# Optimization experiments

Measured on AMD Instinct MI355X. Metric: run time of the kernel, lower is better.

The kernel has to match this reference:

```python
import jax, jax.numpy as jnp
import numpy as np

B, S, V, E, H, M, CS, U = 1, 2048, 50257, 512, 768, 256, 64, 2048


def setup_inputs() -> dict:
    key = jax.random.key(0)
    ks = jax.random.split(key, 16)
    s = 0.02
    p = {}
    p["input_ids"] = jax.random.randint(ks[0], (B, S), 0, V)
    p["untied_token_ids"] = jax.random.randint(ks[1], (U,), 0, V)
    p["emb"] = jax.random.normal(ks[2], (V, E)) * s
    p["w_ih"] = jax.random.normal(ks[3], (3 * H, E)) * s
    p["w_hh"] = jax.random.normal(ks[4], (3 * H, H)) * s
    p["b_ih"] = jnp.zeros((3 * H,))
    p["b_hh"] = jnp.zeros((3 * H,))
    p["Wq"] = jax.random.normal(ks[5], (M, H)) * s
    p["bq"] = jnp.zeros((M,))
    p["Wk"] = jax.random.normal(ks[6], (M, H)) * s
    p["bk"] = jnp.zeros((M,))
    p["Whf"] = jax.random.normal(ks[7], (4 * E, H)) * s
    p["bhf"] = jnp.zeros((4 * E,))
    p["Whp"] = jax.random.normal(ks[8], (E, 4 * E)) * s
    p["bhp"] = jnp.zeros((E,))
    p["Wcv"] = jax.random.normal(ks[9], (E, H)) * s
    p["bcv"] = jnp.zeros((E,))
    p["Wph"] = jax.random.normal(ks[10], (U, E)) * s
    p["bph"] = jnp.zeros((U,))
    p["out_bias"] = jnp.zeros((V,))
    return p


def gru(x, w_ih, w_hh, b_ih, b_hh):
    # x: [B, S, E] -> states [B, S, H]; PyTorch GRU gate order (r, z, n)
    Hh = w_hh.shape[1]

    def step(h, xt):
        gx = xt @ w_ih.T + b_ih
        gh = h @ w_hh.T + b_hh
        xr, xz, xn = jnp.split(gx, 3, axis=-1)
        hr, hz, hn = jnp.split(gh, 3, axis=-1)
        r = jax.nn.sigmoid(xr + hr)
        z = jax.nn.sigmoid(xz + hz)
        n = jnp.tanh(xn + r * hn)
        h = (1.0 - z) * n + z * h
        return h, h

    h0 = jnp.zeros((x.shape[0], Hh), x.dtype)
    _, hs = jax.lax.scan(step, h0, jnp.swapaxes(x, 0, 1))
    return jnp.swapaxes(hs, 0, 1)


def reference(input_ids, untied_token_ids, emb, w_ih, w_hh, b_ih, b_hh, Wq, bq, Wk, bk, Whf, bhf, Whp, bhp, Wcv, bcv, Wph, bph, out_bias):
    x = emb[input_ids]                                  # [B,S,E]
    states = gru(x, w_ih, w_hh, b_ih, b_hh)             # [B,S,H] (dropout=0, eval)
    head = jnp.square(jax.nn.relu(states @ Whf.T + bhf))  # [B,S,4E]
    base_feat = head @ Whp.T + bhp                      # [B,S,E]
    base_logits = base_feat @ emb.T + out_bias          # [B,S,V]

    nc = S // CS  # S == max_length, divisible by chunk_size -> pad_len = 0
    chunked = states.reshape(B, nc, CS, H).mean(axis=2)  # [B,nc,H]
    qk = states @ Wq.T + bq                              # [B,S,M]
    mk = chunked @ Wk.T + bk                             # [B,nc,M]
    scores = jnp.einsum('bsm,bcm->bsc', qk, mk) / jnp.sqrt(jnp.asarray(M, qk.dtype))

    chunk_ends = jnp.minimum(jnp.arange(nc) * CS + (CS - 1), S - 1)
    mask = chunk_ends[None, None, :] < jnp.arange(S)[None, :, None]  # [1,S,nc]
    neg = jnp.finfo(scores.dtype).min
    scores = jnp.where(mask, scores, neg)
    attn = jax.nn.softmax(scores, axis=-1) * mask
    attn = attn / jnp.clip(attn.sum(axis=-1, keepdims=True), 1e-6)

    base_partial = base_feat @ Wph.T + bph               # [B,S,U]
    chunk_partial = (chunked @ Wcv.T + bcv) @ Wph.T + bph  # [B,nc,U]
    mem_partial = jnp.einsum('bsc,bcu->bsu', attn, chunk_partial)
    total_partial = base_partial + mem_partial           # [B,S,U]

    # scatter_add partial logits into full-vocab logits (duplicates accumulate)
    return base_logits.at[:, :, untied_token_ids].add(total_partial)
```

## Files before the change

### kernel.cpp

```cpp
#include <hip/hip_runtime.h>
#include <hip/hip_bf16.h>
#include <math.h>

#define SEQ   2048
#define VOC   50257
#define EMB   512
#define HID   768
#define G3    2304
#define MDIM  256
#define CSZ   64
#define NCHUNK 32
#define UDIM  2048
#define E4    2048

#define G_GRU 48
#define CANARY 0xFFFFFFFFu

typedef uint32_t u32x4  __attribute__((ext_vector_type(4)));
typedef float    f32x4  __attribute__((ext_vector_type(4)));
typedef short    s16x8  __attribute__((ext_vector_type(8)));
typedef __bf16   bf16x8 __attribute__((ext_vector_type(8)));

__global__ __launch_bounds__(256) void cvt_f32_bf16(const float* __restrict__ src,
                                                    __bf16* __restrict__ dst, int n8) {
    int stride = gridDim.x * 256;
    for (int i = blockIdx.x * 256 + threadIdx.x; i < n8; i += stride) {
        const float4* s = reinterpret_cast<const float4*>(src + (size_t)i * 8);
        float4 a = s[0], b = s[1];
        bf16x8 o;
        o[0]=(__bf16)a.x; o[1]=(__bf16)a.y; o[2]=(__bf16)a.z; o[3]=(__bf16)a.w;
        o[4]=(__bf16)b.x; o[5]=(__bf16)b.y; o[6]=(__bf16)b.z; o[7]=(__bf16)b.w;
        *reinterpret_cast<bf16x8*>(dst + (size_t)i * 8) = o;
    }
}

__global__ __launch_bounds__(256) void embed_kernel(const int* __restrict__ ids,
                                                    const float* __restrict__ emb,
                                                    float* __restrict__ X) {
    int s = blockIdx.x;
    int id = ids[s];
    const float* src = &emb[(size_t)id * EMB];
    float* dst = &X[(size_t)s * EMB];
    for (int i = threadIdx.x; i < EMB; i += 256) dst[i] = src[i];
}

__global__ __launch_bounds__(64) void embed16_kernel(const int* __restrict__ ids,
                                                     const __bf16* __restrict__ emb16,
                                                     __bf16* __restrict__ X16) {
    int s = blockIdx.x;
    int id = ids[s];
    const bf16x8* src = reinterpret_cast<const bf16x8*>(emb16 + (size_t)id * EMB);
    bf16x8* dst = reinterpret_cast<bf16x8*>(X16 + (size_t)s * EMB);
    int i = threadIdx.x;
    dst[i] = src[i];
}

template<int EPI>
__global__ __launch_bounds__(256) void gemm_nt(const float* __restrict__ A,
                                               const float* __restrict__ B,
                                               const float* __restrict__ bias,
                                               float* __restrict__ C,
                                               int M, int N, int K) {
    __shared__ float As[16][132];
    __shared__ float Bs[16][132];
    const int tid = threadIdx.x;
    const int tx = tid & 15;
    const int ty = tid >> 4;
    const int m0 = blockIdx.y * 128;
    const int n0 = blockIdx.x * 128;

    float acc[8][8];
    #pragma unroll
    for (int i = 0; i < 8; i++)
        #pragma unroll
        for (int j = 0; j < 8; j++) acc[i][j] = 0.f;

    for (int k0 = 0; k0 < K; k0 += 16) {
        #pragma unroll
        for (int i = 0; i < 2; i++) {
            int idx = tid * 2 + i;
            int r   = idx >> 2;
            int c4  = idx & 3;
            float4 av = {0.f, 0.f, 0.f, 0.f};
            float4 bv = {0.f, 0.f, 0.f, 0.f};
            int ar = m0 + r;
            if (ar < M) av = *reinterpret_cast<const float4*>(&A[(size_t)ar * K + k0 + c4 * 4]);
            int br = n0 + r;
            if (br < N) bv = *reinterpret_cast<const float4*>(&B[(size_t)br * K + k0 + c4 * 4]);
            As[c4 * 4 + 0][r] = av.x; As[c4 * 4 + 1][r] = av.y;
            As[c4 * 4 + 2][r] = av.z; As[c4 * 4 + 3][r] = av.w;
            Bs[c4 * 4 + 0][r] = bv.x; Bs[c4 * 4 + 1][r] = bv.y;
            Bs[c4 * 4 + 2][r] = bv.z; Bs[c4 * 4 + 3][r] = bv.w;
        }
        __syncthreads();
        #pragma unroll
        for (int k = 0; k < 16; k++) {
            float4 a0 = *reinterpret_cast<const float4*>(&As[k][ty * 4]);
            float4 a1 = *reinterpret_cast<const float4*>(&As[k][64 + ty * 4]);
            float4 b0 = *reinterpret_cast<const float4*>(&Bs[k][tx * 4]);
            float4 b1 = *reinterpret_cast<const float4*>(&Bs[k][64 + tx * 4]);
            float a[8] = {a0.x, a0.y, a0.z, a0.w, a1.x, a1.y, a1.z, a1.w};
            float b[8] = {b0.x, b0.y, b0.z, b0.w, b1.x, b1.y, b1.z, b1.w};
            #pragma unroll
            for (int i = 0; i < 8; i++)
                #pragma unroll
                for (int j = 0; j < 8; j++)
                    acc[i][j] = fmaf(a[i], b[j], acc[i][j]);
        }
        __syncthreads();
    }

    #pragma unroll
    for (int i = 0; i < 8; i++) {
        int r = m0 + ((i < 4) ? (ty * 4 + i) : (64 + ty * 4 + (i - 4)));
        if (r >= M) continue;
        #pragma unroll
        for (int j = 0; j < 8; j++) {
            int c = n0 + ((j < 4) ? (tx * 4 + j) : (64 + tx * 4 + (j - 4)));
            if (c >= N) continue;
            float v = acc[i][j] + bias[c];
            if (EPI == 1) { v = fmaxf(v, 0.f); v = v * v; }
            C[(size_t)r * N + c] = v;
        }
    }
}

template<int EPI>
__global__ __launch_bounds__(256) void gemm_bt16(const __bf16* __restrict__ A,
                                                 const __bf16* __restrict__ B,
                                                 const float* __restrict__ bias,
                                                 float* __restrict__ C,
                                                 int M, int N, int K) {
    constexpr int LDT = 40;
    __shared__ __bf16 As[128 * LDT];
    __shared__ __bf16 Bs[128 * LDT];
    const int tid  = threadIdx.x;
    const int lane = tid & 63;
    const int wave = tid >> 6;
    const int wm = wave >> 1;
    const int wn = wave & 1;
    const int m0 = blockIdx.y * 128;
    const int n0 = blockIdx.x * 128;
    const int l15 = lane & 15;
    const int l4  = lane >> 4;

    f32x4 acc[4][4];
    #pragma unroll
    for (int i = 0; i < 4; i++)
        #pragma unroll
        for (int j = 0; j < 4; j++) acc[i][j] = (f32x4){0.f, 0.f, 0.f, 0.f};

    const int r  = tid >> 1;
    const int hf = tid & 1;

    for (int k0 = 0; k0 < K; k0 += 32) {
        const __bf16* ap = &A[(size_t)(m0 + r) * K + k0 + hf * 16];
        s16x8 av0 = *reinterpret_cast<const s16x8*>(ap);
        s16x8 av1 = *reinterpret_cast<const s16x8*>(ap + 8);
        s16x8 bv0, bv1;
        #pragma unroll
        for (int q = 0; q < 8; q++) { bv0[q] = 0; bv1[q] = 0; }
        int bn = n0 + r;
        if (bn < N) {
            const __bf16* bp = &B[(size_t)bn * K + k0 + hf * 16];
            bv0 = *reinterpret_cast<const s16x8*>(bp);
            bv1 = *reinterpret_cast<const s16x8*>(bp + 8);
        }
        __syncthreads();
        *reinterpret_cast<s16x8*>(&As[r * LDT + hf * 16])     = av0;
        *reinterpret_cast<s16x8*>(&As[r * LDT + hf * 16 + 8]) = av1;
        *reinterpret_cast<s16x8*>(&Bs[r * LDT + hf * 16])     = bv0;
        *reinterpret_cast<s16x8*>(&Bs[r * LDT + hf * 16 + 8]) = bv1;
        __syncthreads();

        s16x8 af[4], bf[4];
        #pragma unroll
        for (int i = 0; i < 4; i++)
            af[i] = *reinterpret_cast<const s16x8*>(&As[(wm * 64 + i * 16 + l15) * LDT + l4 * 8]);
        #pragma unroll
        for (int j = 0; j < 4; j++)
            bf[j] = *reinterpret_cast<const s16x8*>(&Bs[(wn * 64 + j * 16 + l15) * LDT + l4 * 8]);
        #pragma unroll
        for (int i = 0; i < 4; i++)
            #pragma unroll
            for (int j = 0; j < 4; j++)
                acc[i][j] = __builtin_amdgcn_mfma_f32_16x16x32_bf16(af[i], bf[j], acc[i][j], 0, 0, 0);
    }

    #pragma unroll
    for (int j = 0; j < 4; j++) {
        int col = n0 + wn * 64 + j * 16 + l15;
        if (col >= N) continue;
        float bv = bias[col];
        #pragma unroll
        for (int i = 0; i < 4; i++) {
            int row = m0 + wm * 64 + i * 16 + l4 * 4;
            #pragma unroll
            for (int q = 0; q < 4; q++) {
                float v = acc[i][j][q] + bv;
                if (EPI == 1) { v = fmaxf(v, 0.f); v = v * v; }
                C[(size_t)(row + q) * N + col] = v;
            }
        }
    }
}

__global__ __launch_bounds__(256) void gemm_bf16_logits(const float* __restrict__ A,
                                                        const float* __restrict__ B,
                                                        const float* __restrict__ bias,
                                                        float* __restrict__ C,
                                                        int M, int N, int K) {
    constexpr int LDT = 40;
    __shared__ __bf16 As[128 * LDT];
    __shared__ __bf16 Bs[128 * LDT];
    const int tid  = threadIdx.x;
    const int lane = tid & 63;
    const int wave = tid >> 6;
    const int wm = wave >> 1;
    const int wn = wave & 1;
    const int m0 = blockIdx.y * 128;
    const int n0 = blockIdx.x * 128;
    const int l15 = lane & 15;
    const int l4  = lane >> 4;

    f32x4 acc[4][4];
    #pragma unroll
    for (int i = 0; i < 4; i++)
        #pragma unroll
        for (int j = 0; j < 4; j++) acc[i][j] = (f32x4){0.f, 0.f, 0.f, 0.f};

    const int r  = tid >> 1;
    const int hf = tid & 1;

    for (int k0 = 0; k0 < K; k0 += 32) {
        const float* ap = &A[(size_t)(m0 + r) * K + k0 + hf * 16];
        float4 a0 = *reinterpret_cast<const float4*>(ap);
        float4 a1 = *reinterpret_cast<const float4*>(ap + 4);
        float4 a2 = *reinterpret_cast<const float4*>(ap + 8);
        float4 a3 = *reinterpret_cast<const float4*>(ap + 12);
        int bn = n0 + r;
        float4 b0 = {0,0,0,0}, b1 = {0,0,0,0}, b2 = {0,0,0,0}, b3 = {0,0,0,0};
        if (bn < N) {
            const float* bp = &B[(size_t)bn * K + k0 + hf * 16];
            b0 = *reinterpret_cast<const float4*>(bp);
            b1 = *reinterpret_cast<const float4*>(bp + 4);
            b2 = *reinterpret_cast<const float4*>(bp + 8);
            b3 = *reinterpret_cast<const float4*>(bp + 12);
        }
        __syncthreads();
        {
            __bf16* da = &As[r * LDT + hf * 16];
            bf16x8 w0, w1;
            w0[0]=(__bf16)a0.x; w0[1]=(__bf16)a0.y; w0[2]=(__bf16)a0.z; w0[3]=(__bf16)a0.w;
            w0[4]=(__bf16)a1.x; w0[5]=(__bf16)a1.y; w0[6]=(__bf16)a1.z; w0[7]=(__bf16)a1.w;
            w1[0]=(__bf16)a2.x; w1[1]=(__bf16)a2.y; w1[2]=(__bf16)a2.z; w1[3]=(__bf16)a2.w;
            w1[4]=(__bf16)a3.x; w1[5]=(__bf16)a3.y; w1[6]=(__bf16)a3.z; w1[7]=(__bf16)a3.w;
            *reinterpret_cast<bf16x8*>(da)     = w0;
            *reinterpret_cast<bf16x8*>(da + 8) = w1;
            __bf16* db = &Bs[r * LDT + hf * 16];
            bf16x8 v0, v1;
            v0[0]=(__bf16)b0.x; v0[1]=(__bf16)b0.y; v0[2]=(__bf16)b0.z; v0[3]=(__bf16)b0.w;
            v0[4]=(__bf16)b1.x; v0[5]=(__bf16)b1.y; v0[6]=(__bf16)b1.z; v0[7]=(__bf16)b1.w;
            v1[0]=(__bf16)b2.x; v1[1]=(__bf16)b2.y; v1[2]=(__bf16)b2.z; v1[3]=(__bf16)b2.w;
            v1[4]=(__bf16)b3.x; v1[5]=(__bf16)b3.y; v1[6]=(__bf16)b3.z; v1[7]=(__bf16)b3.w;
            *reinterpret_cast<bf16x8*>(db)     = v0;
            *reinterpret_cast<bf16x8*>(db + 8) = v1;
        }
        __syncthreads();

        s16x8 af[4], bf[4];
        #pragma unroll
        for (int i = 0; i < 4; i++)
            af[i] = *reinterpret_cast<const s16x8*>(&As[(wm * 64 + i * 16 + l15) * LDT + l4 * 8]);
        #pragma unroll
        for (int j = 0; j < 4; j++)
            bf[j] = *reinterpret_cast<const s16x8*>(&Bs[(wn * 64 + j * 16 + l15) * LDT + l4 * 8]);
        #pragma unroll
        for (int i = 0; i < 4; i++)
            #pragma unroll
            for (int j = 0; j < 4; j++)
                acc[i][j] = __builtin_amdgcn_mfma_f32_16x16x32_bf16(af[i], bf[j], acc[i][j], 0, 0, 0);
    }

    #pragma unroll
    for (int j = 0; j < 4; j++) {
        int col = n0 + wn * 64 + j * 16 + l15;
        if (col >= N) continue;
        float bv = bias[col];
        #pragma unroll
        for (int i = 0; i < 4; i++) {
            int row = m0 + wm * 64 + i * 16 + l4 * 4;
            #pragma unroll
            for (int q = 0; q < 4; q++)
                C[(size_t)(row + q) * N + col] = acc[i][j][q] + bv;
        }
    }
}

__device__ __forceinline__ float fast_sigmoid(float x) {
    x = fminf(fmaxf(x, -30.f), 30.f);
    return __builtin_amdgcn_rcpf(1.f + __expf(-x));
}
__device__ __forceinline__ float fast_tanh(float x) {
    x = fminf(fmaxf(x, -15.f), 15.f);
    float e = __expf(2.f * x);
    return (e - 1.f) * __builtin_amdgcn_rcpf(e + 1.f);
}

__global__ __launch_bounds__(256, 1) void gru_kernel(const float* __restrict__ GX,
                                                     const float* __restrict__ Whh,
                                                     const float* __restrict__ bhh,
                                                     float* __restrict__ states) {
    __shared__ float h_s[HID];
    const int tid  = threadIdx.x;
    const int g    = blockIdx.x;
    const int tx   = tid & 15;
    const int ty   = tid >> 4;
    const int gu   = g * 16 + ty;
    const int wave = tid >> 6;
    const int lane = tid & 63;

    float4 W4[3][12];
    #pragma unroll
    for (int p = 0; p < 3; p++) {
        const float* wr = &Whh[(size_t)(p * HID + gu) * HID + 4 * tx];
        #pragma unroll
        for (int j = 0; j < 12; j++)
            W4[p][j] = *reinterpret_cast<const float4*>(&wr[64 * j]);
    }
    float bh[3];
    #pragma unroll
    for (int p = 0; p < 3; p++) bh[p] = bhh[p * HID + gu];

    float hv  = 0.f;
    float gx0 = GX[0 * HID + gu];
    float gx1 = GX[1 * HID + gu];
    float gx2 = GX[2 * HID + gu];

    for (int t = 0; t < SEQ; t++) {
        float ngx0 = 0.f, ngx1 = 0.f, ngx2 = 0.f;
        if (t + 1 < SEQ) {
            const float* gp = &GX[(size_t)(t + 1) * G3];
            ngx0 = gp[0 * HID + gu];
            ngx1 = gp[1 * HID + gu];
            ngx2 = gp[2 * HID + gu];
        }

        float4 h4[12];
        if (t > 0) {
            if (tid < 192) {
                const float* pp = states + (size_t)(t - 1) * HID + tid * 4;
                u32x4 q;
                float s;
                do {
                    asm volatile(
                        "global_load_dwordx4 %0, %1, off sc0 sc1\n\t"
                        "s_waitcnt vmcnt(0)"
                        : "=&v"(q) : "v"(pp) : "memory");
                    f32x4 f = __builtin_bit_cast(f32x4, q);
                    s = f[0] + f[1] + f[2] + f[3];
                } while (s != s);
                *reinterpret_cast<u32x4*>(&h_s[tid * 4]) = q;
            }
            __syncthreads();
            #pragma unroll
            for (int j = 0; j < 12; j++)
                h4[j] = *reinterpret_cast<const float4*>(&h_s[4 * tx + 64 * j]);
        } else {
            #pragma unroll
            for (int j = 0; j < 12; j++) h4[j] = make_float4(0.f, 0.f, 0.f, 0.f);
        }

        float accp[3];
        #pragma unroll
        for (int p = 0; p < 3; p++) {
            float a = 0.f;
            #pragma unroll
            for (int j = 0; j < 12; j++) {
                a = fmaf(W4[p][j].x, h4[j].x, a);
                a = fmaf(W4[p][j].y, h4[j].y, a);
                a = fmaf(W4[p][j].z, h4[j].z, a);
                a = fmaf(W4[p][j].w, h4[j].w, a);
            }
            accp[p] = a;
        }
        #pragma unroll
        for (int p = 0; p < 3; p++) {
            accp[p] += __shfl_xor(accp[p], 1);
            accp[p] += __shfl_xor(accp[p], 2);
            accp[p] += __shfl_xor(accp[p], 4);
            accp[p] += __shfl_xor(accp[p], 8);
        }

        float r = fast_sigmoid(gx0 + accp[0] + bh[0]);
        float z = fast_sigmoid(gx1 + accp[1] + bh[1]);
        float n = fast_tanh(gx2 + r * (accp[2] + bh[2]));
        hv = (1.f - z) * n + z * hv;

        float v0 = __shfl(hv, 0);
        float v1 = __shfl(hv, 16);
        float v2 = __shfl(hv, 32);
        float v3 = __shfl(hv, 48);
        if (lane == 0) {
            f32x4 pv = {v0, v1, v2, v3};
            float* dp = states + (size_t)t * HID + g * 16 + wave * 4;
            asm volatile(
                "global_store_dwordx4 %0, %1, off sc0 sc1"
                :: "v"(dp), "v"(pv) : "memory");
        }
        gx0 = ngx0; gx1 = ngx1; gx2 = ngx2;
    }
}

__global__ __launch_bounds__(256) void chunkmean_kernel(const float* __restrict__ states,
                                                        float* __restrict__ chunked) {
    int c = blockIdx.x;
    for (int e = threadIdx.x; e < HID; e += 256) {
        float s = 0.f;
        #pragma unroll 8
        for (int i = 0; i < CSZ; i++)
            s += states[(size_t)(c * CSZ + i) * HID + e];
        chunked[c * HID + e] = s * (1.f / 64.f);
    }
}

__global__ void attn_kernel(const float* __restrict__ qk,
                            const float* __restrict__ mk,
                            float* __restrict__ attn) {
    int s = blockIdx.x;
    int lane = threadIdx.x;
    int c = lane & 31;
    int h = lane >> 5;
    const float* q = &qk[(size_t)s * MDIM];
    const float* m = &mk[(size_t)c * MDIM];
    float sc = 0.f;
    for (int k = h; k < MDIM; k += 2) sc = fmaf(q[k], m[k], sc);
    sc += __shfl_xor(sc, 32);
    sc *= (1.0f / 16.0f);
    bool allowed = (CSZ * c + (CSZ - 1)) < s;
    float v = allowed ? sc : -3.4e38f;
    float mx = v;
    #pragma unroll
    for (int d = 16; d >= 1; d >>= 1) mx = fmaxf(mx, __shfl_xor(mx, d));
    float e = (allowed && mx > -1e37f) ? expf(sc - mx) : 0.f;
    float sm = e;
    #pragma unroll
    for (int d = 16; d >= 1; d >>= 1) sm += __shfl_xor(sm, d);
    float a = (sm > 0.f) ? e / sm : 0.f;
    if (lane < 32) attn[(size_t)s * NCHUNK + c] = a;
}

__global__ __launch_bounds__(256) void total_scatter_kernel(const float* __restrict__ bp,
                                                            const float* __restrict__ cp,
                                                            const float* __restrict__ attn,
                                                            const int* __restrict__ uids,
                                                            float* __restrict__ out) {
    int s = blockIdx.x;
    __shared__ float a_s[NCHUNK];
    if (threadIdx.x < NCHUNK) a_s[threadIdx.x] = attn[(size_t)s * NCHUNK + threadIdx.x];
    __syncthreads();
    for (int u = threadIdx.x; u < UDIM; u += 256) {
        float t = bp[(size_t)s * UDIM + u];
        #pragma unroll 8
        for (int c = 0; c < NCHUNK; c++)
            t = fmaf(a_s[c], cp[(size_t)c * UDIM + u], t);
        atomicAdd(&out[(size_t)s * VOC + uids[u]], t);
    }
}

static inline int cvt_grid(int n8) {
    int g = (n8 + 255) / 256;
    return g > 2048 ? 2048 : g;
}

extern "C" void kernel_launch(void* const* d_in, const int* in_sizes, int n_in,
                              void* d_out, int out_size, void* d_ws, size_t ws_size,
                              hipStream_t stream) {
    const int*   ids   = (const int*)d_in[0];
    const int*   uids  = (const int*)d_in[1];
    const float* emb   = (const float*)d_in[2];
    const float* w_ih  = (const float*)d_in[3];
    const float* w_hh  = (const float*)d_in[4];
    const float* b_ih  = (const float*)d_in[5];
    const float* b_hh  = (const float*)d_in[6];
    const float* Wq    = (const float*)d_in[7];
    const float* bq    = (const float*)d_in[8];
    const float* Wk    = (const float*)d_in[9];
    const float* bk    = (const float*)d_in[10];
    const float* Whf   = (const float*)d_in[11];
    const float* bhf   = (const float*)d_in[12];
    const float* Whp   = (const float*)d_in[13];
    const float* bhp   = (const float*)d_in[14];
    const float* Wcv   = (const float*)d_in[15];
    const float* bcv   = (const float*)d_in[16];
    const float* Wph   = (const float*)d_in[17];
    const float* bph   = (const float*)d_in[18];
    const float* obias = (const float*)d_in[19];
    float* out = (float*)d_out;
    float* wsf = (float*)d_ws;

    size_t off = 0;
    float* GX     = wsf + off; off += (size_t)SEQ * G3;
    float* states = wsf + off; off += (size_t)SEQ * HID;
    float* head   = wsf + off; off += (size_t)SEQ * E4;
    float* bfeat  = wsf + off; off += (size_t)SEQ * EMB;
    float* chunk  = wsf + off; off += (size_t)NCHUNK * HID;
    float* qk     = wsf + off; off += (size_t)SEQ * MDIM;
    float* mk     = wsf + off; off += (size_t)NCHUNK * MDIM;
    float* cv     = wsf + off; off += (size_t)NCHUNK * EMB;
    float* cp     = wsf + off; off += (size_t)NCHUNK * UDIM;
    float* bp     = wsf + off; off += (size_t)SEQ * UDIM;
    float* attn   = wsf + off; off += (size_t)SEQ * NCHUNK;
    size_t common_off = off;

    __bf16* X16     = (__bf16*)(wsf + off); off += (size_t)SEQ * EMB / 2;
    __bf16* emb16   = (__bf16*)(wsf + off); off += (size_t)VOC * EMB / 2;
    __bf16* wih16   = (__bf16*)(wsf + off); off += (size_t)G3 * EMB / 2;
    __bf16* Whp16   = (__bf16*)(wsf + off); off += (size_t)EMB * E4 / 2;
    __bf16* Wph16   = (__bf16*)(wsf + off); off += (size_t)UDIM * EMB / 2;
    __bf16* head16  = (__bf16*)(wsf + off); off += (size_t)SEQ * E4 / 2;
    __bf16* bfeat16 = (__bf16*)(wsf + off); off += (size_t)SEQ * EMB / 2;
    const bool big = ws_size >= off * sizeof(float);

    if (big) {
        cvt_f32_bf16<<<cvt_grid(VOC * EMB / 8), 256, 0, stream>>>(emb, emb16, VOC * EMB / 8);
        cvt_f32_bf16<<<cvt_grid(G3 * EMB / 8), 256, 0, stream>>>(w_ih, wih16, G3 * EMB / 8);
        cvt_f32_bf16<<<cvt_grid(EMB * E4 / 8), 256, 0, stream>>>(Whp, Whp16, EMB * E4 / 8);
        cvt_f32_bf16<<<cvt_grid(UDIM * EMB / 8), 256, 0, stream>>>(Wph, Wph16, UDIM * EMB / 8);
        embed16_kernel<<<SEQ, 64, 0, stream>>>(ids, emb16, X16);
        hipMemsetAsync(states, 0xFF, (size_t)SEQ * HID * sizeof(float), stream);
        gemm_bt16<0><<<dim3(G3 / 128, SEQ / 128), 256, 0, stream>>>(X16, wih16, b_ih, GX, SEQ, G3, EMB);
        gru_kernel<<<G_GRU, 256, 0, stream>>>(GX, w_hh, b_hh, states);
        chunkmean_kernel<<<NCHUNK, 256, 0, stream>>>(states, chunk);
        gemm_nt<0><<<dim3(MDIM / 128, SEQ / 128), 256, 0, stream>>>(states, Wq, bq, qk, SEQ, MDIM, HID);
        gemm_nt<0><<<dim3(MDIM / 128, 1), 256, 0, stream>>>(chunk, Wk, bk, mk, NCHUNK, MDIM, HID);
        gemm_nt<1><<<dim3(E4 / 128, SEQ / 128), 256, 0, stream>>>(states, Whf, bhf, head, SEQ, E4, HID);
        cvt_f32_bf16<<<cvt_grid(SEQ * E4 / 8), 256, 0, stream>>>(head, head16, SEQ * E4 / 8);
        gemm_bt16<0><<<dim3(EMB / 128, SEQ / 128), 256, 0, stream>>>(head16, Whp16, bhp, bfeat, SEQ, EMB, E4);
        cvt_f32_bf16<<<cvt_grid(SEQ * EMB / 8), 256, 0, stream>>>(bfeat, bfeat16, SEQ * EMB / 8);
        gemm_nt<0><<<dim3(EMB / 128, 1), 256, 0, stream>>>(chunk, Wcv, bcv, cv, NCHUNK, EMB, HID);
        gemm_nt<0><<<dim3(UDIM / 128, 1), 256, 0, stream>>>(cv, Wph, bph, cp, NCHUNK, UDIM, EMB);
        gemm_bt16<0><<<dim3(UDIM / 128, SEQ / 128), 256, 0, stream>>>(bfeat16, Wph16, bph, bp, SEQ, UDIM, EMB);
        gemm_bt16<0><<<dim3((VOC + 127) / 128, SEQ / 128), 256, 0, stream>>>(bfeat16, emb16, obias, out, SEQ, VOC, EMB);
        attn_kernel<<<SEQ, 64, 0, stream>>>(qk, mk, attn);
        total_scatter_kernel<<<SEQ, 256, 0, stream>>>(bp, cp, attn, uids, out);
    } else {
        float* X = wsf + common_off;
        embed_kernel<<<SEQ, 256, 0, stream>>>(ids, emb, X);
        hipMemsetAsync(states, 0xFF, (size_t)SEQ * HID * sizeof(float), stream);
        gemm_nt<0><<<dim3(G3 / 128, SEQ / 128), 256, 0, stream>>>(X, w_ih, b_ih, GX, SEQ, G3, EMB);
        gru_kernel<<<G_GRU, 256, 0, stream>>>(GX, w_hh, b_hh, states);
        chunkmean_kernel<<<NCHUNK, 256, 0, stream>>>(states, chunk);
        gemm_nt<0><<<dim3(MDIM / 128, SEQ / 128), 256, 0, stream>>>(states, Wq, bq, qk, SEQ, MDIM, HID);
        gemm_nt<0><<<dim3(MDIM / 128, 1), 256, 0, stream>>>(chunk, Wk, bk, mk, NCHUNK, MDIM, HID);
        gemm_nt<1><<<dim3(E4 / 128, SEQ / 128), 256, 0, stream>>>(states, Whf, bhf, head, SEQ, E4, HID);
        gemm_nt<0><<<dim3(EMB / 128, SEQ / 128), 256, 0, stream>>>(head, Whp, bhp, bfeat, SEQ, EMB, E4);
        gemm_nt<0><<<dim3(EMB / 128, 1), 256, 0, stream>>>(chunk, Wcv, bcv, cv, NCHUNK, EMB, HID);
        gemm_nt<0><<<dim3(UDIM / 128, 1), 256, 0, stream>>>(cv, Wph, bph, cp, NCHUNK, UDIM, EMB);
        gemm_nt<0><<<dim3(UDIM / 128, SEQ / 128), 256, 0, stream>>>(bfeat, Wph, bph, bp, SEQ, UDIM, EMB);
        gemm_bf16_logits<<<dim3((VOC + 127) / 128, SEQ / 128), 256, 0, stream>>>(bfeat, emb, obias, out, SEQ, VOC, EMB);
        attn_kernel<<<SEQ, 64, 0, stream>>>(qk, mk, attn);
        total_scatter_kernel<<<SEQ, 256, 0, stream>>>(bp, cp, attn, uids, out);
    }
}
```

Baseline: 5.172 ms.

## Overlap GRU recurrence with downstream head and logits GEMMs in a persistent mega-kernel

Merges the GRU recurrence, head projection, feature projection, vocab logits GEMM and base_partial GEMM into one persistent kernel. GRU blocks write states while consumer blocks poll on NaN-canary state rows and atomic stage flags, then compute 128-row stages of the downstream GEMMs as soon as their inputs are ready. Intermediate head and bfeat outputs are written directly as bf16, dropping the separate conversion kernels. The aim is to hide the serial GRU latency behind the large logits GEMM. The cost is spin-waiting, reliance on all 256 blocks being co-resident, and GEMM blocks competing with GRU blocks for bandwidth.

```diff
diff --git a/kernel.cpp b/kernel.cpp
--- a/kernel.cpp
+++ b/kernel.cpp
@@ -14,6 +14,8 @@
 #define E4    2048
 
 #define G_GRU 48
+#define NCONS 208
+#define NSTAGE 16
 #define CANARY 0xFFFFFFFFu
 
 typedef uint32_t u32x4  __attribute__((ext_vector_type(4)));
@@ -125,24 +127,18 @@
     }
 }
 
-template<int EPI>
-__global__ __launch_bounds__(256) void gemm_bt16(const __bf16* __restrict__ A,
-                                                 const __bf16* __restrict__ B,
-                                                 const float* __restrict__ bias,
-                                                 float* __restrict__ C,
-                                                 int M, int N, int K) {
+template<bool A16, bool B16, int EPI, bool OUT16>
+__device__ void mfma_tile(const void* Ap, const void* Bp,
+                          const float* __restrict__ bias, void* Cp,
+                          int m0, int n0, int N, int K,
+                          __bf16* As, __bf16* Bs) {
     constexpr int LDT = 40;
-    __shared__ __bf16 As[128 * LDT];
-    __shared__ __bf16 Bs[128 * LDT];
     const int tid  = threadIdx.x;
     const int lane = tid & 63;
     const int wave = tid >> 6;
-    const int wm = wave >> 1;
-    const int wn = wave & 1;
-    const int m0 = blockIdx.y * 128;
-    const int n0 = blockIdx.x * 128;
-    const int l15 = lane & 15;
-    const int l4  = lane >> 4;
+    const int wm = wave >> 1, wn = wave & 1;
+    const int l15 = lane & 15, l4 = lane >> 4;
+    const int r = tid >> 1, hf = tid & 1;
 
     f32x4 acc[4][4];
     #pragma unroll
@@ -150,21 +146,51 @@
         #pragma unroll
         for (int j = 0; j < 4; j++) acc[i][j] = (f32x4){0.f, 0.f, 0.f, 0.f};
 
-    const int r  = tid >> 1;
-    const int hf = tid & 1;
-
     for (int k0 = 0; k0 < K; k0 += 32) {
-        const __bf16* ap = &A[(size_t)(m0 + r) * K + k0 + hf * 16];
-        s16x8 av0 = *reinterpret_cast<const s16x8*>(ap);
-        s16x8 av1 = *reinterpret_cast<const s16x8*>(ap + 8);
-        s16x8 bv0, bv1;
-        #pragma unroll
-        for (int q = 0; q < 8; q++) { bv0[q] = 0; bv1[q] = 0; }
+        s16x8 av0, av1, bv0, bv1;
+        if constexpr (A16) {
+            const __bf16* ap = (const __bf16*)Ap + (size_t)(m0 + r) * K + k0 + hf * 16;
+            av0 = *reinterpret_cast<const s16x8*>(ap);
+            av1 = *reinterpret_cast<const s16x8*>(ap + 8);
+        } else {
+            const float* ap = (const float*)Ap + (size_t)(m0 + r) * K + k0 + hf * 16;
+            float4 a0 = *reinterpret_cast<const float4*>(ap);
+            float4 a1 = *reinterpret_cast<const float4*>(ap + 4);
+            float4 a2 = *reinterpret_cast<const float4*>(ap + 8);
+            float4 a3 = *reinterpret_cast<const float4*>(ap + 12);
+            bf16x8 w0, w1;
+            w0[0]=(__bf16)a0.x; w0[1]=(__bf16)a0.y; w0[2]=(__bf16)a0.z; w0[3]=(__bf16)a0.w;
+            w0[4]=(__bf16)a1.x; w0[5]=(__bf16)a1.y; w0[6]=(__bf16)a1.z; w0[7]=(__bf16)a1.w;
+            w1[0]=(__bf16)a2.x; w1[1]=(__bf16)a2.y; w1[2]=(__bf16)a2.z; w1[3]=(__bf16)a2.w;
+            w1[4]=(__bf16)a3.x; w1[5]=(__bf16)a3.y; w1[6]=(__bf16)a3.z; w1[7]=(__bf16)a3.w;
+            av0 = __builtin_bit_cast(s16x8, w0); av1 = __builtin_bit_cast(s16x8, w1);
+        }
         int bn = n0 + r;
-        if (bn < N) {
-            const __bf16* bp = &B[(size_t)bn * K + k0 + hf * 16];
-            bv0 = *reinterpret_cast<const s16x8*>(bp);
-            bv1 = *reinterpret_cast<const s16x8*>(bp + 8);
+        if constexpr (B16) {
+            if (bn < N) {
+                const __bf16* bp2 = (const __bf16*)Bp + (size_t)bn * K + k0 + hf * 16;
+                bv0 = *reinterpret_cast<const s16x8*>(bp2);
+                bv1 = *reinterpret_cast<const s16x8*>(bp2 + 8);
+            } else {
+                bv0 = (s16x8){0,0,0,0,0,0,0,0}; bv1 = (s16x8){0,0,0,0,0,0,0,0};
+            }
+        } else {
+            bf16x8 v0, v1;
+            if (bn < N) {
+                const float* bp2 = (const float*)Bp + (size_t)bn * K + k0 + hf * 16;
+                float4 b0 = *reinterpret_cast<const float4*>(bp2);
+                float4 b1 = *reinterpret_cast<const float4*>(bp2 + 4);
+                float4 b2 = *reinterpret_cast<const float4*>(bp2 + 8);
+                float4 b3 = *reinterpret_cast<const float4*>(bp2 + 12);
+                v0[0]=(__bf16)b0.x; v0[1]=(__bf16)b0.y; v0[2]=(__bf16)b0.z; v0[3]=(__bf16)b0.w;
+                v0[4]=(__bf16)b1.x; v0[5]=(__bf16)b1.y; v0[6]=(__bf16)b1.z; v0[7]=(__bf16)b1.w;
+                v1[0]=(__bf16)b2.x; v1[1]=(__bf16)b2.y; v1[2]=(__bf16)b2.z; v1[3]=(__bf16)b2.w;
+                v1[4]=(__bf16)b3.x; v1[5]=(__bf16)b3.y; v1[6]=(__bf16)b3.z; v1[7]=(__bf16)b3.w;
+            } else {
+                #pragma unroll
+                for (int q = 0; q < 8; q++) { v0[q] = (__bf16)0.f; v1[q] = (__bf16)0.f; }
+            }
+            bv0 = __builtin_bit_cast(s16x8, v0); bv1 = __builtin_bit_cast(s16x8, v1);
         }
         __syncthreads();
         *reinterpret_cast<s16x8*>(&As[r * LDT + hf * 16])     = av0;
@@ -199,102 +225,49 @@
             for (int q = 0; q < 4; q++) {
                 float v = acc[i][j][q] + bv;
                 if (EPI == 1) { v = fmaxf(v, 0.f); v = v * v; }
-                C[(size_t)(row + q) * N + col] = v;
+                if constexpr (OUT16)
+                    ((__bf16*)Cp)[(size_t)(row + q) * N + col] = (__bf16)v;
+                else
+                    ((float*)Cp)[(size_t)(row + q) * N + col] = v;
             }
         }
     }
 }
 
-__global__ __launch_bounds__(256) void gemm_bf16_logits(const float* __restrict__ A,
-                                                        const float* __restrict__ B,
-                                                        const float* __restrict__ bias,
-                                                        float* __restrict__ C,
-                                                        int M, int N, int K) {
-    constexpr int LDT = 40;
-    __shared__ __bf16 As[128 * LDT];
-    __shared__ __bf16 Bs[128 * LDT];
-    const int tid  = threadIdx.x;
-    const int lane = tid & 63;
-    const int wave = tid >> 6;
-    const int wm = wave >> 1;
-    const int wn = wave & 1;
-    const int m0 = blockIdx.y * 128;
-    const int n0 = blockIdx.x * 128;
-    const int l15 = lane & 15;
-    const int l4  = lane >> 4;
-
-    f32x4 acc[4][4];
-    #pragma unroll
-    for (int i = 0; i < 4; i++)
-        #pragma unroll
-        for (int j = 0; j < 4; j++) acc[i][j] = (f32x4){0.f, 0.f, 0.f, 0.f};
-
-    const int r  = tid >> 1;
-    const int hf = tid & 1;
-
-    for (int k0 = 0; k0 < K; k0 += 32) {
-        const float* ap = &A[(size_t)(m0 + r) * K + k0 + hf * 16];
-        float4 a0 = *reinterpret_cast<const float4*>(ap);
-        float4 a1 = *reinterpret_cast<const float4*>(ap + 4);
-        float4 a2 = *reinterpret_cast<const float4*>(ap + 8);
-        float4 a3 = *reinterpret_cast<const float4*>(ap + 12);
-        int bn = n0 + r;
-        float4 b0 = {0,0,0,0}, b1 = {0,0,0,0}, b2 = {0,0,0,0}, b3 = {0,0,0,0};
-        if (bn < N) {
-            const float* bp = &B[(size_t)bn * K + k0 + hf * 16];
-            b0 = *reinterpret_cast<const float4*>(bp);
-            b1 = *reinterpret_cast<const float4*>(bp + 4);
-            b2 = *reinterpret_cast<const float4*>(bp + 8);
-            b3 = *reinterpret_cast<const float4*>(bp + 12);
-        }
-        __syncthreads();
-        {
-            __bf16* da = &As[r * LDT + hf * 16];
-            bf16x8 w0, w1;
-            w0[0]=(__bf16)a0.x; w0[1]=(__bf16)a0.y; w0[2]=(__bf16)a0.z; w0[3]=(__bf16)a0.w;
-            w0[4]=(__bf16)a1.x; w0[5]=(__bf16)a1.y; w0[6]=(__bf16)a1.z; w0[7]=(__bf16)a1.w;
-            w1[0]=(__bf16)a2.x; w1[1]=(__bf16)a2.y; w1[2]=(__bf16)a2.z; w1[3]=(__bf16)a2.w;
-            w1[4]=(__bf16)a3.x; w1[5]=(__bf16)a3.y; w1[6]=(__bf16)a3.z; w1[7]=(__bf16)a3.w;
-            *reinterpret_cast<bf16x8*>(da)     = w0;
-            *reinterpret_cast<bf16x8*>(da + 8) = w1;
-            __bf16* db = &Bs[r * LDT + hf * 16];
-            bf16x8 v0, v1;
-            v0[0]=(__bf16)b0.x; v0[1]=(__bf16)b0.y; v0[2]=(__bf16)b0.z; v0[3]=(__bf16)b0.w;
-            v0[4]=(__bf16)b1.x; v0[5]=(__bf16)b1.y; v0[6]=(__bf16)b1.z; v0[7]=(__bf16)b1.w;
-            v1[0]=(__bf16)b2.x; v1[1]=(__bf16)b2.y; v1[2]=(__bf16)b2.z; v1[3]=(__bf16)b2.w;
-            v1[4]=(__bf16)b3.x; v1[5]=(__bf16)b3.y; v1[6]=(__bf16)b3.z; v1[7]=(__bf16)b3.w;
-            *reinterpret_cast<bf16x8*>(db)     = v0;
-            *reinterpret_cast<bf16x8*>(db + 8) = v1;
-        }
-        __syncthreads();
-
-        s16x8 af[4], bf[4];
-        #pragma unroll
-        for (int i = 0; i < 4; i++)
-            af[i] = *reinterpret_cast<const s16x8*>(&As[(wm * 64 + i * 16 + l15) * LDT + l4 * 8]);
-        #pragma unroll
-        for (int j = 0; j < 4; j++)
-            bf[j] = *reinterpret_cast<const s16x8*>(&Bs[(wn * 64 + j * 16 + l15) * LDT + l4 * 8]);
-        #pragma unroll
-        for (int i = 0; i < 4; i++)
-            #pragma unroll
-            for (int j = 0; j < 4; j++)
-                acc[i][j] = __builtin_amdgcn_mfma_f32_16x16x32_bf16(af[i], bf[j], acc[i][j], 0, 0, 0);
-    }
-
-    #pragma unroll
-    for (int j = 0; j < 4; j++) {
-        int col = n0 + wn * 64 + j * 16 + l15;
-        if (col >= N) continue;
-        float bv = bias[col];
-        #pragma unroll
-        for (int i = 0; i < 4; i++) {
-            int row = m0 + wm * 64 + i * 16 + l4 * 4;
-            #pragma unroll
-            for (int q = 0; q < 4; q++)
-                C[(size_t)(row + q) * N + col] = acc[i][j][q] + bv;
-        }
-    }
+__global__ __launch_bounds__(256) void gemm_bt16_k(const __bf16* A, const __bf16* B,
+                                                   const float* bias, float* C,
+                                                   int N, int K) {
+    __shared__ __bf16 lds[2 * 128 * 40];
+    mfma_tile<true, true, 0, false>(A, B, bias, C, blockIdx.y * 128, blockIdx.x * 128,
+                                    N, K, lds, lds + 128 * 40);
+}
+
+__global__ __launch_bounds__(256) void gemm_bf16_logits(const float* A, const float* B,
+                                                        const float* bias, float* C,
+                                                        int N, int K) {
+    __shared__ __bf16 lds[2 * 128 * 40];
+    mfma_tile<false, false, 0, false>(A, B, bias, C, blockIdx.y * 128, blockIdx.x * 128,
+                                      N, K, lds, lds + 128 * 40);
+}
+
+__device__ void poll_row(const float* row, const unsigned* acq) {
+    if (threadIdx.x < 192) {
+        const float* pp = row + threadIdx.x * 4;
+        u32x4 q;
+        float s;
+        do {
+            asm volatile(
+                "global_load_dwordx4 %0, %1, off sc0 sc1\n\t"
+                "s_waitcnt vmcnt(0)"
+                : "=&v"(q) : "v"(pp) : "memory");
+            f32x4 f = __builtin_bit_cast(f32x4, q);
+            s = f[0] + f[1] + f[2] + f[3];
+        } while (s != s);
+    }
+    __syncthreads();
+    if (threadIdx.x == 0)
+        (void)__hip_atomic_load(acq, __ATOMIC_ACQUIRE, __HIP_MEMORY_SCOPE_AGENT);
+    __syncthreads();
 }
 
 __device__ __forceinline__ float fast_sigmoid(float x) {
@@ -307,13 +280,12 @@
     return (e - 1.f) * __builtin_amdgcn_rcpf(e + 1.f);
 }
 
-__global__ __launch_bounds__(256, 1) void gru_kernel(const float* __restrict__ GX,
-                                                     const float* __restrict__ Whh,
-                                                     const float* __restrict__ bhh,
-                                                     float* __restrict__ states) {
-    __shared__ float h_s[HID];
+__device__ void gru_body(const float* __restrict__ GX,
+                         const float* __restrict__ Whh,
+                         const float* __restrict__ bhh,
+                         float* __restrict__ states,
+                         float* h_s, int g) {
     const int tid  = threadIdx.x;
-    const int g    = blockIdx.x;
     const int tx   = tid & 15;
     const int ty   = tid >> 4;
     const int gu   = g * 16 + ty;
@@ -409,6 +381,71 @@
                 :: "v"(dp), "v"(pv) : "memory");
         }
         gx0 = ngx0; gx1 = ngx1; gx2 = ngx2;
+    }
+}
+
+__global__ __launch_bounds__(256, 1) void gru_kernel(const float* GX, const float* Whh,
+                                                     const float* bhh, float* states) {
+    __shared__ float h_s[HID];
+    gru_body(GX, Whh, bhh, states, h_s, blockIdx.x);
+}
+
+__global__ __launch_bounds__(256, 1) void mega_kernel(
+        const float* __restrict__ GX, const float* __restrict__ Whh,
+        const float* __restrict__ bhh, float* __restrict__ states,
+        const float* __restrict__ Whf, const float* __restrict__ bhf,
+        __bf16* __restrict__ head16,
+        const __bf16* __restrict__ Whp16, const float* __restrict__ bhp,
+        __bf16* __restrict__ bfeat16,
+        const __bf16* __restrict__ emb16, const float* __restrict__ obias,
+        float* __restrict__ out,
+        const __bf16* __restrict__ Wph16, const float* __restrict__ bph,
+        float* __restrict__ bp,
+        unsigned* __restrict__ flags) {
+    __shared__ __bf16 lds[2 * 128 * 40];
+
+    if (blockIdx.x < G_GRU) {
+        gru_body(GX, Whh, bhh, states, (float*)lds, blockIdx.x);
+        return;
+    }
+
+    const int w = blockIdx.x - G_GRU;
+    __bf16* As = lds;
+    __bf16* Bs = lds + 128 * 40;
+    unsigned* head_done  = flags;
+    unsigned* bfeat_done = flags + 16;
+    const unsigned* acq  = flags + 32;
+
+    for (int i = 0; i < NSTAGE; i++) {
+        const int m0 = 128 * i;
+        if (w < 16) {
+            poll_row(states + (size_t)(m0 + 127) * HID, acq);
+            mfma_tile<false, false, 1, true>(states, Whf, bhf, head16,
+                                             m0, 128 * w, E4, HID, As, Bs);
+            __syncthreads();
+            if (threadIdx.x == 0)
+                __hip_atomic_fetch_add(&head_done[i], 1u, __ATOMIC_RELEASE, __HIP_MEMORY_SCOPE_AGENT);
+        }
+        if (w < 4) {
+            if (threadIdx.x == 0)
+                while (__hip_atomic_load(&head_done[i], __ATOMIC_ACQUIRE, __HIP_MEMORY_SCOPE_AGENT) < 16u) {}
+            __syncthreads();
+            mfma_tile<true, true, 0, true>(head16, Whp16, bhp, bfeat16,
+                                           m0, 128 * w, EMB, E4, As, Bs);
+            __syncthreads();
+            if (threadIdx.x == 0)
+                __hip_atomic_fetch_add(&bfeat_done[i], 1u, __ATOMIC_RELEASE, __HIP_MEMORY_SCOPE_AGENT);
+        }
+        if (threadIdx.x == 0)
+            while (__hip_atomic_load(&bfeat_done[i], __ATOMIC_ACQUIRE, __HIP_MEMORY_SCOPE_AGENT) < 4u) {}
+        __syncthreads();
+        for (int t = w; t < 393; t += NCONS)
+            mfma_tile<true, true, 0, false>(bfeat16, emb16, obias, out,
+                                            m0, 128 * t, VOC, EMB, As, Bs);
+        if (w >= 192)
+            mfma_tile<true, true, 0, false>(bfeat16, Wph16, bph, bp,
+                                            m0, 128 * (w - 192), UDIM, EMB, As, Bs);
+        __syncthreads();
     }
 }
 
@@ -520,6 +557,7 @@
     __bf16* Wph16   = (__bf16*)(wsf + off); off += (size_t)UDIM * EMB / 2;
     __bf16* head16  = (__bf16*)(wsf + off); off += (size_t)SEQ * E4 / 2;
     __bf16* bfeat16 = (__bf16*)(wsf + off); off += (size_t)SEQ * EMB / 2;
+    unsigned* flags = (unsigned*)(wsf + off); off += 64;
     const bool big = ws_size >= off * sizeof(float);
 
     if (big) {
@@ -529,19 +567,16 @@
         cvt_f32_bf16<<<cvt_grid(UDIM * EMB / 8), 256, 0, stream>>>(Wph, Wph16, UDIM * EMB / 8);
         embed16_kernel<<<SEQ, 64, 0, stream>>>(ids, emb16, X16);
         hipMemsetAsync(states, 0xFF, (size_t)SEQ * HID * sizeof(float), stream);
-        gemm_bt16<0><<<dim3(G3 / 128, SEQ / 128), 256, 0, stream>>>(X16, wih16, b_ih, GX, SEQ, G3, EMB);
-        gru_kernel<<<G_GRU, 256, 0, stream>>>(GX, w_hh, b_hh, states);
+        hipMemsetAsync(flags, 0, 64 * sizeof(unsigned), stream);
+        gemm_bt16_k<<<dim3(G3 / 128, SEQ / 128), 256, 0, stream>>>(X16, wih16, b_ih, GX, G3, EMB);
+        mega_kernel<<<G_GRU + NCONS, 256, 0, stream>>>(
+            GX, w_hh, b_hh, states, Whf, bhf, head16, Whp16, bhp, bfeat16,
+            emb16, obias, out, Wph16, bph, bp, flags);
         chunkmean_kernel<<<NCHUNK, 256, 0, stream>>>(states, chunk);
         gemm_nt<0><<<dim3(MDIM / 128, SEQ / 128), 256, 0, stream>>>(states, Wq, bq, qk, SEQ, MDIM, HID);
         gemm_nt<0><<<dim3(MDIM / 128, 1), 256, 0, stream>>>(chunk, Wk, bk, mk, NCHUNK, MDIM, HID);
-        gemm_nt<1><<<dim3(E4 / 128, SEQ / 128), 256, 0, stream>>>(states, Whf, bhf, head, SEQ, E4, HID);
-        cvt_f32_bf16<<<cvt_grid(SEQ * E4 / 8), 256, 0, stream>>>(head, head16, SEQ * E4 / 8);
-        gemm_bt16<0><<<dim3(EMB / 128, SEQ / 128), 256, 0, stream>>>(head16, Whp16, bhp, bfeat, SEQ, EMB, E4);
-        cvt_f32_bf16<<<cvt_grid(SEQ * EMB / 8), 256, 0, stream>>>(bfeat, bfeat16, SEQ * EMB / 8);
         gemm_nt<0><<<dim3(EMB / 128, 1), 256, 0, stream>>>(chunk, Wcv, bcv, cv, NCHUNK, EMB, HID);
         gemm_nt<0><<<dim3(UDIM / 128, 1), 256, 0, stream>>>(cv, Wph, bph, cp, NCHUNK, UDIM, EMB);
-        gemm_bt16<0><<<dim3(UDIM / 128, SEQ / 128), 256, 0, stream>>>(bfeat16, Wph16, bph, bp, SEQ, UDIM, EMB);
-        gemm_bt16<0><<<dim3((VOC + 127) / 128, SEQ / 128), 256, 0, stream>>>(bfeat16, emb16, obias, out, SEQ, VOC, EMB);
         attn_kernel<<<SEQ, 64, 0, stream>>>(qk, mk, attn);
         total_scatter_kernel<<<SEQ, 256, 0, stream>>>(bp, cp, attn, uids, out);
     } else {
@@ -558,7 +593,7 @@
         gemm_nt<0><<<dim3(EMB / 128, 1), 256, 0, stream>>>(chunk, Wcv, bcv, cv, NCHUNK, EMB, HID);
         gemm_nt<0><<<dim3(UDIM / 128, 1), 256, 0, stream>>>(cv, Wph, bph, cp, NCHUNK, UDIM, EMB);
         gemm_nt<0><<<dim3(UDIM / 128, SEQ / 128), 256, 0, stream>>>(bfeat, Wph, bph, bp, SEQ, UDIM, EMB);
-        gemm_bf16_logits<<<dim3((VOC + 127) / 128, SEQ / 128), 256, 0, stream>>>(bfeat, emb, obias, out, SEQ, VOC, EMB);
+        gemm_bf16_logits<<<dim3((VOC + 127) / 128, SEQ / 128), 256, 0, stream>>>(bfeat, emb, obias, out, VOC, EMB);
         attn_kernel<<<SEQ, 64, 0, stream>>>(qk, mk, attn);
         total_scatter_kernel<<<SEQ, 256, 0, stream>>>(bp, cp, attn, uids, out);
     }
```

New measurement: 8.356 ms. 61.6% more time.
